# Kernel tuning notes

Measured on AMD Instinct MI355X. Metric: run time of the kernel, lower is better.

The kernel has to match this reference:

```python
import jax, jax.numpy as jnp
import numpy as np

N_ITEM_SRC = 100000
N_ITEM_DST = 50000
N_USER0 = 50000
N_USER1 = 25000
E_II = 800000
E_IU0 = 800000
E_IU1 = 400000
D_IN = 256
D_H = 256
D_OUT = 128


def setup_inputs() -> dict:
    key = jax.random.key(0)
    ks = jax.random.split(key, 16)
    f = jnp.float32
    s = 0.05  # weight init scale
    return {
        "x_item": jax.random.normal(ks[0], (N_ITEM_SRC, D_IN), f),
        "x_user": jax.random.normal(ks[1], (N_USER0, D_H), f),
        "src_ii": jax.random.randint(ks[2], (E_II,), 0, N_ITEM_SRC, jnp.int32),
        "dst_ii": jax.random.randint(ks[3], (E_II,), 0, N_ITEM_DST, jnp.int32),
        "src_iu0": jax.random.randint(ks[4], (E_IU0,), 0, N_ITEM_SRC, jnp.int32),
        "dst_iu0": jax.random.randint(ks[5], (E_IU0,), 0, N_USER0, jnp.int32),
        "src_iu1": jax.random.randint(ks[6], (E_IU1,), 0, N_ITEM_DST, jnp.int32),
        "dst_iu1": jax.random.randint(ks[7], (E_IU1,), 0, N_USER1, jnp.int32),
        "Wn1": jax.random.normal(ks[8], (D_IN, D_H), f) * s,
        "Ws1": jax.random.normal(ks[9], (D_IN, D_H), f) * s,
        "b1": jnp.zeros((D_H,), f),
        "Wn2": jax.random.normal(ks[10], (D_H, D_H), f) * s,
        "Ws2": jax.random.normal(ks[11], (D_H, D_H), f) * s,
        "b2": jnp.zeros((D_H,), f),
        "Wn3": jax.random.normal(ks[12], (D_H, D_H), f) * s,
        "Ws3": jax.random.normal(ks[13], (D_H, D_H), f) * s,
        "b3": jnp.zeros((D_H,), f),
        "Wlin": jax.random.normal(ks[14], (D_H, D_OUT), f) * s,
        "blin": jnp.zeros((D_OUT,), f),
        "n_item_dst": N_ITEM_DST,
        "n_user1": N_USER1,
    }


def _sage_mean(x_src, x_dst, src, dst, n_dst, Wn, Ws, b):
    """DGL SAGEConv('mean'): fc_self(x_dst) + fc_neigh(mean_{in-nbrs} x_src) + bias.
    Isolated dst nodes get zero neighbor contribution (clamp degree to 1)."""
    deg = jax.ops.segment_sum(jnp.ones(dst.shape, x_src.dtype), dst, num_segments=n_dst)
    agg = jax.ops.segment_sum(x_src[src], dst, num_segments=n_dst)  # [n_dst, d]
    agg = agg / jnp.maximum(deg, 1.0)[:, None]
    return x_dst @ Ws + agg @ Wn + b


def reference(x_item, x_user, src_ii, dst_ii, src_iu0, dst_iu0, src_iu1, dst_iu1,
              Wn1, Ws1, b1, Wn2, Ws2, b2, Wn3, Ws3, b3, Wlin, blin,
              n_item_dst, n_user1):
    # conv1: item->item (block: dst item feats are prefix of src item feats)
    item_x = jax.nn.relu(_sage_mean(x_item, x_item[:n_item_dst], src_ii, dst_ii,
                                    n_item_dst, Wn1, Ws1, b1))
    # conv2: item->user at hop 0
    user_x = jax.nn.relu(_sage_mean(x_item, x_user, src_iu0, dst_iu0,
                                    x_user.shape[0], Wn2, Ws2, b2))
    user_x = user_x[:n_user1]
    # conv3: item->user at hop 1
    user_x = jax.nn.relu(_sage_mean(item_x, user_x, src_iu1, dst_iu1,
                                    n_user1, Wn3, Ws3, b3))
    return user_x @ Wlin + blin
```

## Files before the change

kernel.cpp:

```cpp
#include <hip/hip_runtime.h>

#define D 256
#define NI_SRC 100000
#define NI_DST 50000
#define NU1 25000
#define EII 800000
#define EIU0 800000
#define EIU1 400000
#define DOUT 128
#define CAP 60

typedef __bf16 bf16x8 __attribute__((ext_vector_type(8)));
typedef float f32x4 __attribute__((ext_vector_type(4)));

__device__ __forceinline__ unsigned short f2bf(float x) {
    unsigned u = __builtin_bit_cast(unsigned, x);
    u += 0x7FFFu + ((u >> 16) & 1u);
    return (unsigned short)(u >> 16);
}
__device__ __forceinline__ float bflo(unsigned u) { return __builtin_bit_cast(float, u << 16); }
__device__ __forceinline__ float bfhi(unsigned u) { return __builtin_bit_cast(float, u & 0xFFFF0000u); }

__global__ __launch_bounds__(256) void cvt_kernel(const float* __restrict__ in,
                                                  unsigned short* __restrict__ out, long n8) {
    long i = (long)blockIdx.x * blockDim.x + threadIdx.x;
    if (i >= n8) return;
    const float4 f1 = *reinterpret_cast<const float4*>(in + i * 8);
    const float4 f2 = *reinterpret_cast<const float4*>(in + i * 8 + 4);
    uint4 v;
    v.x = f2bf(f1.x) | ((unsigned)f2bf(f1.y) << 16);
    v.y = f2bf(f1.z) | ((unsigned)f2bf(f1.w) << 16);
    v.z = f2bf(f2.x) | ((unsigned)f2bf(f2.y) << 16);
    v.w = f2bf(f2.z) | ((unsigned)f2bf(f2.w) << 16);
    *reinterpret_cast<uint4*>(out + i * 8) = v;
}

__global__ __launch_bounds__(256) void wcvt_all(const float* __restrict__ W0, const float* __restrict__ W1,
                                                const float* __restrict__ W2, const float* __restrict__ W3,
                                                const float* __restrict__ W4, const float* __restrict__ W5,
                                                const float* __restrict__ W6,
                                                unsigned short* __restrict__ out) {
    int t = blockIdx.x * blockDim.x + threadIdx.x;
    const float* W; int NN; int base;
    if (t < 393216) {
        int w = t >> 16; base = w << 16;
        W = (w == 0) ? W0 : (w == 1) ? W1 : (w == 2) ? W2 : (w == 3) ? W3 : (w == 4) ? W4 : W5;
        NN = 256;
    } else if (t < 425984) { base = 393216; W = W6; NN = 128; }
    else return;
    int i = t - base;
    int n = i >> 8, k = i & 255;
    out[t] = f2bf(W[(size_t)k * NN + n]);
}

__global__ void bucket_all(const int* __restrict__ s1, const int* __restrict__ d1,
                           int* __restrict__ u1, int* __restrict__ e1,
                           const int* __restrict__ s2, const int* __restrict__ d2,
                           int* __restrict__ u2, int* __restrict__ e2,
                           const int* __restrict__ s3, const int* __restrict__ d3,
                           int* __restrict__ u3, int* __restrict__ e3) {
    int i0 = blockIdx.x * blockDim.x + threadIdx.x;
    int stride = gridDim.x * blockDim.x;
    for (int i = i0; i < EII; i += stride) {
        int d = d1[i]; int p = atomicAdd(&u1[d], 1);
        if (p < CAP) e1[d * CAP + p] = s1[i];
    }
    for (int i = i0; i < EIU0; i += stride) {
        int d = d2[i];
        if (d < NU1) { int p = atomicAdd(&u2[d], 1); if (p < CAP) e2[d * CAP + p] = s2[i]; }
    }
    for (int i = i0; i < EIU1; i += stride) {
        int d = d3[i]; int p = atomicAdd(&u3[d], 1);
        if (p < CAP) e3[d * CAP + p] = s3[i];
    }
}

__global__ __launch_bounds__(256) void gather_cap(const unsigned short* __restrict__ X,
                                                  const int* __restrict__ csr,
                                                  const int* __restrict__ cnt,
                                                  unsigned short* __restrict__ out, int nrows) {
    int wid = (blockIdx.x * blockDim.x + threadIdx.x) >> 6;
    int lane = threadIdx.x & 63;
    if (wid >= nrows) return;
    int c = min(cnt[wid], CAP);
    const int s = wid * CAP;
    const int half = lane >> 5;
    const int l32 = lane & 31;
    float acc[8] = {};
    for (int j = 0; j < c; j += 64) {
        int myid = (j + lane < c) ? csr[s + j + lane] : 0;
        int rem = min(64, c - j);
        int tmax = min(32, rem);
        for (int t = 0; t < tmax; ++t) {
            int idx = t + half * 32;
            int sid = __shfl(myid, idx, 64);
            if (idx < rem) {
                const uint4 v = *reinterpret_cast<const uint4*>(X + (size_t)sid * D + l32 * 8);
                acc[0] += bflo(v.x); acc[1] += bfhi(v.x);
                acc[2] += bflo(v.y); acc[3] += bfhi(v.y);
                acc[4] += bflo(v.z); acc[5] += bfhi(v.z);
                acc[6] += bflo(v.w); acc[7] += bfhi(v.w);
            }
        }
    }
#pragma unroll
    for (int q = 0; q < 8; ++q) acc[q] += __shfl_xor(acc[q], 32, 64);
    if (half == 0) {
        float r = 1.0f / fmaxf((float)c, 1.0f);
        uint4 o;
        o.x = f2bf(acc[0] * r) | ((unsigned)f2bf(acc[1] * r) << 16);
        o.y = f2bf(acc[2] * r) | ((unsigned)f2bf(acc[3] * r) << 16);
        o.z = f2bf(acc[4] * r) | ((unsigned)f2bf(acc[5] * r) << 16);
        o.w = f2bf(acc[6] * r) | ((unsigned)f2bf(acc[7] * r) << 16);
        *reinterpret_cast<uint4*>(out + (size_t)wid * D + l32 * 8) = o;
    }
}

template<bool A1F32, bool HAS_AGG, bool RELU, bool OUTF32>
__global__ __launch_bounds__(256) void sage_gemm(
    const unsigned short* __restrict__ A1b, const float* __restrict__ A1f,
    const unsigned short* __restrict__ A2,
    const unsigned short* __restrict__ W1t, const unsigned short* __restrict__ W2t,
    const float* __restrict__ bias,
    unsigned short* __restrict__ Cb, float* __restrict__ Cf,
    int M, int N)
{
    __shared__ unsigned short sA[128 * 40];
    __shared__ unsigned short sB[128 * 40];
    const int tid = threadIdx.x;
    const int lane = tid & 63;
    const int wid = tid >> 6;
    const int wrow = (wid >> 1) * 64;
    const int wcol = (wid & 1) * 64;
    const int brow = blockIdx.x * 128;
    const int bcol = blockIdx.y * 128;

    f32x4 acc[4][4] = {};

    const int r0 = tid >> 2;
    const int k0 = (tid & 3) * 8;

    const int nPass = HAS_AGG ? 2 : 1;
    for (int pass = 0; pass < nPass; ++pass) {
        const unsigned short* __restrict__ Wt = pass ? W2t : W1t;
        for (int kt = 0; kt < 256; kt += 32) {
#pragma unroll
            for (int c = 0; c < 2; ++c) {
                int row = r0 + c * 64;
                int grow = brow + row;
                uint4 val = {0u, 0u, 0u, 0u};
                if (pass == 0) {
                    if (A1F32) {
                        if (grow < M) {
                            const float4 f1 = *reinterpret_cast<const float4*>(A1f + (size_t)grow * 256 + kt + k0);
                            const float4 f2 = *reinterpret_cast<const float4*>(A1f + (size_t)grow * 256 + kt + k0 + 4);
                            val.x = f2bf(f1.x) | ((unsigned)f2bf(f1.y) << 16);
                            val.y = f2bf(f1.z) | ((unsigned)f2bf(f1.w) << 16);
                            val.z = f2bf(f2.x) | ((unsigned)f2bf(f2.y) << 16);
                            val.w = f2bf(f2.z) | ((unsigned)f2bf(f2.w) << 16);
                        }
                    } else {
                        if (grow < M) val = *reinterpret_cast<const uint4*>(A1b + (size_t)grow * 256 + kt + k0);
                    }
                } else {
                    if (grow < M) val = *reinterpret_cast<const uint4*>(A2 + (size_t)grow * 256 + kt + k0);
                }
                *reinterpret_cast<uint4*>(sA + row * 40 + k0) = val;
                *reinterpret_cast<uint4*>(sB + row * 40 + k0) =
                    *reinterpret_cast<const uint4*>(Wt + (size_t)(bcol + row) * 256 + kt + k0);
            }
            __syncthreads();
            const int fr = lane & 15;
            const int fk = (lane >> 4) * 8;
            bf16x8 af[4], bfr[4];
#pragma unroll
            for (int f = 0; f < 4; ++f) {
                af[f]  = __builtin_bit_cast(bf16x8, *reinterpret_cast<const uint4*>(sA + (wrow + f * 16 + fr) * 40 + fk));
                bfr[f] = __builtin_bit_cast(bf16x8, *reinterpret_cast<const uint4*>(sB + (wcol + f * 16 + fr) * 40 + fk));
            }
#pragma unroll
            for (int mi = 0; mi < 4; ++mi)
#pragma unroll
                for (int ni = 0; ni < 4; ++ni)
                    acc[mi][ni] = __builtin_amdgcn_mfma_f32_16x16x32_bf16(af[mi], bfr[ni], acc[mi][ni], 0, 0, 0);
            __syncthreads();
        }
    }

    const int cr = (lane >> 4) * 4;
    const int cc = lane & 15;
#pragma unroll
    for (int mi = 0; mi < 4; ++mi) {
#pragma unroll
        for (int j = 0; j < 4; ++j) {
            int grow = brow + wrow + mi * 16 + cr + j;
            if (grow >= M) continue;
#pragma unroll
            for (int ni = 0; ni < 4; ++ni) {
                int gcol = bcol + wcol + ni * 16 + cc;
                float v = acc[mi][ni][j] + bias[gcol];
                if (RELU) v = fmaxf(v, 0.f);
                if (OUTF32) Cf[(size_t)grow * N + gcol] = v;
                else Cb[(size_t)grow * N + gcol] = f2bf(v);
            }
        }
    }
}

extern "C" void kernel_launch(void* const* d_in, const int* in_sizes, int n_in,
                              void* d_out, int out_size, void* d_ws, size_t ws_size,
                              hipStream_t stream) {
    const float* x_item = (const float*)d_in[0];
    const float* x_user = (const float*)d_in[1];
    const int* src_ii  = (const int*)d_in[2];
    const int* dst_ii  = (const int*)d_in[3];
    const int* src_iu0 = (const int*)d_in[4];
    const int* dst_iu0 = (const int*)d_in[5];
    const int* src_iu1 = (const int*)d_in[6];
    const int* dst_iu1 = (const int*)d_in[7];
    const float* Wn1 = (const float*)d_in[8];
    const float* Ws1 = (const float*)d_in[9];
    const float* b1  = (const float*)d_in[10];
    const float* Wn2 = (const float*)d_in[11];
    const float* Ws2 = (const float*)d_in[12];
    const float* b2  = (const float*)d_in[13];
    const float* Wn3 = (const float*)d_in[14];
    const float* Ws3 = (const float*)d_in[15];
    const float* b3  = (const float*)d_in[16];
    const float* Wlin = (const float*)d_in[17];
    const float* blin = (const float*)d_in[18];
    float* out = (float*)d_out;

    unsigned short* xb_item = (unsigned short*)d_ws;
    unsigned short* aggbuf  = xb_item + (size_t)NI_SRC * D;
    unsigned short* item_x  = aggbuf + (size_t)NI_DST * D;
    unsigned short* wts     = item_x + (size_t)NI_DST * D;
    unsigned short* overlay = wts + 425984;

    unsigned short* user_x2 = overlay;
    int* cur1 = (int*)overlay;
    int* cur2 = cur1 + 50000;
    int* cur3 = cur2 + 25000;
    int* csr1 = cur3 + 25000;
    int* csr2 = csr1 + 50000 * CAP;
    int* csr3 = csr2 + 25000 * CAP;

    unsigned short* Wt_s1 = wts;
    unsigned short* Wt_n1 = wts + 65536;
    unsigned short* Wt_s2 = wts + 2 * 65536;
    unsigned short* Wt_n2 = wts + 3 * 65536;
    unsigned short* Wt_s3 = wts + 4 * 65536;
    unsigned short* Wt_n3 = wts + 5 * 65536;
    unsigned short* Wt_li = wts + 6 * 65536;

    unsigned short* agg2 = aggbuf;
    unsigned short* agg3 = aggbuf + (size_t)NU1 * D;
    unsigned short* user_x3 = aggbuf;

    long n8 = (long)NI_SRC * D / 8;
    cvt_kernel<<<(int)((n8 + 255) / 256), 256, 0, stream>>>(x_item, xb_item, n8);
    wcvt_all<<<1664, 256, 0, stream>>>(Ws1, Wn1, Ws2, Wn2, Ws3, Wn3, Wlin, wts);

    hipMemsetAsync(cur1, 0, sizeof(int) * 100000, stream);
    bucket_all<<<512, 256, 0, stream>>>(src_ii, dst_ii, cur1, csr1,
                                        src_iu0, dst_iu0, cur2, csr2,
                                        src_iu1, dst_iu1, cur3, csr3);

    dim3 g1((NI_DST + 127) / 128, 2);
    dim3 g2((NU1 + 127) / 128, 2);
    dim3 g4((NU1 + 127) / 128, 1);

    gather_cap<<<(NI_DST * 64 + 255) / 256, 256, 0, stream>>>(xb_item, csr1, cur1, aggbuf, NI_DST);
    sage_gemm<false, true, true, false><<<g1, 256, 0, stream>>>(
        xb_item, nullptr, aggbuf, Wt_s1, Wt_n1, b1, item_x, nullptr, NI_DST, D);

    gather_cap<<<(NU1 * 64 + 255) / 256, 256, 0, stream>>>(xb_item, csr2, cur2, agg2, NU1);
    gather_cap<<<(NU1 * 64 + 255) / 256, 256, 0, stream>>>(item_x, csr3, cur3, agg3, NU1);

    sage_gemm<true, true, true, false><<<g2, 256, 0, stream>>>(
        nullptr, x_user, agg2, Wt_s2, Wt_n2, b2, user_x2, nullptr, NU1, D);

    sage_gemm<false, true, true, false><<<g2, 256, 0, stream>>>(
        user_x2, nullptr, agg3, Wt_s3, Wt_n3, b3, user_x3, nullptr, NU1, D);

    sage_gemm<false, false, false, true><<<g4, 256, 0, stream>>>(
        user_x3, nullptr, nullptr, Wt_li, nullptr, blin, nullptr, out, NU1, DOUT);
}
```

Measured before the change: 389.6 us.

## Merge independent prep, gather and GEMM stages into combined launches

Three preprocessing kernels (edge bucketing, weight transpose-convert and feature bf16 conversion) become one block-partitioned prep kernel, and the bucketing now loads edges eight at a time with int4 loads. The conv1 and conv2 neighbour gathers are merged into one launch, and so are their two GEMMs. Conv1's self term now reads the fp32 features directly. Workspace buffers are re-overlaid so the merged stages can share memory. The aim is fewer launches and less tail idle time between small dependent kernels, at the cost of uneven work mixes inside a single grid.

```diff
diff --git a/kernel.cpp b/kernel.cpp
--- a/kernel.cpp
+++ b/kernel.cpp
@@ -10,6 +10,14 @@
 #define DOUT 128
 #define CAP 60
 
+#define NB_BUCKET 512
+#define NB_WCVT 1664
+#define NB_CVT 12500
+#define NGRP1 100000
+#define NGRP2 100000
+#define NGRP3 50000
+#define NGRP 250000
+
 typedef __bf16 bf16x8 __attribute__((ext_vector_type(8)));
 typedef float f32x4 __attribute__((ext_vector_type(4)));
 
@@ -21,66 +29,67 @@
 __device__ __forceinline__ float bflo(unsigned u) { return __builtin_bit_cast(float, u << 16); }
 __device__ __forceinline__ float bfhi(unsigned u) { return __builtin_bit_cast(float, u & 0xFFFF0000u); }
 
-__global__ __launch_bounds__(256) void cvt_kernel(const float* __restrict__ in,
-                                                  unsigned short* __restrict__ out, long n8) {
-    long i = (long)blockIdx.x * blockDim.x + threadIdx.x;
-    if (i >= n8) return;
-    const float4 f1 = *reinterpret_cast<const float4*>(in + i * 8);
-    const float4 f2 = *reinterpret_cast<const float4*>(in + i * 8 + 4);
-    uint4 v;
-    v.x = f2bf(f1.x) | ((unsigned)f2bf(f1.y) << 16);
-    v.y = f2bf(f1.z) | ((unsigned)f2bf(f1.w) << 16);
-    v.z = f2bf(f2.x) | ((unsigned)f2bf(f2.y) << 16);
-    v.w = f2bf(f2.z) | ((unsigned)f2bf(f2.w) << 16);
-    *reinterpret_cast<uint4*>(out + i * 8) = v;
-}
-
-__global__ __launch_bounds__(256) void wcvt_all(const float* __restrict__ W0, const float* __restrict__ W1,
-                                                const float* __restrict__ W2, const float* __restrict__ W3,
-                                                const float* __restrict__ W4, const float* __restrict__ W5,
-                                                const float* __restrict__ W6,
-                                                unsigned short* __restrict__ out) {
-    int t = blockIdx.x * blockDim.x + threadIdx.x;
-    const float* W; int NN; int base;
-    if (t < 393216) {
-        int w = t >> 16; base = w << 16;
-        W = (w == 0) ? W0 : (w == 1) ? W1 : (w == 2) ? W2 : (w == 3) ? W3 : (w == 4) ? W4 : W5;
-        NN = 256;
-    } else if (t < 425984) { base = 393216; W = W6; NN = 128; }
-    else return;
-    int i = t - base;
-    int n = i >> 8, k = i & 255;
-    out[t] = f2bf(W[(size_t)k * NN + n]);
-}
-
-__global__ void bucket_all(const int* __restrict__ s1, const int* __restrict__ d1,
-                           int* __restrict__ u1, int* __restrict__ e1,
-                           const int* __restrict__ s2, const int* __restrict__ d2,
-                           int* __restrict__ u2, int* __restrict__ e2,
-                           const int* __restrict__ s3, const int* __restrict__ d3,
-                           int* __restrict__ u3, int* __restrict__ e3) {
-    int i0 = blockIdx.x * blockDim.x + threadIdx.x;
-    int stride = gridDim.x * blockDim.x;
-    for (int i = i0; i < EII; i += stride) {
-        int d = d1[i]; int p = atomicAdd(&u1[d], 1);
-        if (p < CAP) e1[d * CAP + p] = s1[i];
-    }
-    for (int i = i0; i < EIU0; i += stride) {
-        int d = d2[i];
-        if (d < NU1) { int p = atomicAdd(&u2[d], 1); if (p < CAP) e2[d * CAP + p] = s2[i]; }
-    }
-    for (int i = i0; i < EIU1; i += stride) {
-        int d = d3[i]; int p = atomicAdd(&u3[d], 1);
-        if (p < CAP) e3[d * CAP + p] = s3[i];
-    }
-}
-
-__global__ __launch_bounds__(256) void gather_cap(const unsigned short* __restrict__ X,
-                                                  const int* __restrict__ csr,
-                                                  const int* __restrict__ cnt,
-                                                  unsigned short* __restrict__ out, int nrows) {
-    int wid = (blockIdx.x * blockDim.x + threadIdx.x) >> 6;
-    int lane = threadIdx.x & 63;
+__device__ __forceinline__ void bucket8(const int* __restrict__ src, const int* __restrict__ dst,
+                                        int* __restrict__ cur, int* __restrict__ csr, int g, int dmax) {
+    const int4 da = reinterpret_cast<const int4*>(dst)[g * 2];
+    const int4 db = reinterpret_cast<const int4*>(dst)[g * 2 + 1];
+    const int4 sa = reinterpret_cast<const int4*>(src)[g * 2];
+    const int4 sb = reinterpret_cast<const int4*>(src)[g * 2 + 1];
+    int d[8] = {da.x, da.y, da.z, da.w, db.x, db.y, db.z, db.w};
+    int s[8] = {sa.x, sa.y, sa.z, sa.w, sb.x, sb.y, sb.z, sb.w};
+    int p[8];
+#pragma unroll
+    for (int q = 0; q < 8; ++q) p[q] = (d[q] < dmax) ? atomicAdd(&cur[d[q]], 1) : CAP;
+#pragma unroll
+    for (int q = 0; q < 8; ++q) if (p[q] < CAP) csr[d[q] * CAP + p[q]] = s[q];
+}
+
+__global__ __launch_bounds__(256) void prep_kernel(
+    const int* __restrict__ s1, const int* __restrict__ d1, int* __restrict__ u1, int* __restrict__ e1,
+    const int* __restrict__ s2, const int* __restrict__ d2, int* __restrict__ u2, int* __restrict__ e2,
+    const int* __restrict__ s3, const int* __restrict__ d3, int* __restrict__ u3, int* __restrict__ e3,
+    const float* __restrict__ W0, const float* __restrict__ W1, const float* __restrict__ W2,
+    const float* __restrict__ W3, const float* __restrict__ W4, const float* __restrict__ W5,
+    const float* __restrict__ W6, unsigned short* __restrict__ wout,
+    const float* __restrict__ xin, unsigned short* __restrict__ xout)
+{
+    int b = blockIdx.x;
+    if (b < NB_BUCKET) {
+        int t0 = b * 256 + threadIdx.x;
+        for (int g = t0; g < NGRP; g += NB_BUCKET * 256) {
+            if (g < NGRP1) bucket8(s1, d1, u1, e1, g, NI_DST);
+            else if (g < NGRP1 + NGRP2) bucket8(s2, d2, u2, e2, g - NGRP1, NU1);
+            else bucket8(s3, d3, u3, e3, g - NGRP1 - NGRP2, NU1);
+        }
+    } else if (b < NB_BUCKET + NB_WCVT) {
+        int t = (b - NB_BUCKET) * 256 + threadIdx.x;
+        const float* W; int NN; int base;
+        if (t < 393216) {
+            int w = t >> 16; base = w << 16;
+            W = (w == 0) ? W0 : (w == 1) ? W1 : (w == 2) ? W2 : (w == 3) ? W3 : (w == 4) ? W4 : W5;
+            NN = 256;
+        } else { base = 393216; W = W6; NN = 128; }
+        int i = t - base;
+        int n = i >> 8, k = i & 255;
+        wout[t] = f2bf(W[(size_t)k * NN + n]);
+    } else {
+        long i = (long)(b - NB_BUCKET - NB_WCVT) * 256 + threadIdx.x;
+        const float4 f1 = *reinterpret_cast<const float4*>(xin + i * 8);
+        const float4 f2 = *reinterpret_cast<const float4*>(xin + i * 8 + 4);
+        uint4 v;
+        v.x = f2bf(f1.x) | ((unsigned)f2bf(f1.y) << 16);
+        v.y = f2bf(f1.z) | ((unsigned)f2bf(f1.w) << 16);
+        v.z = f2bf(f2.x) | ((unsigned)f2bf(f2.y) << 16);
+        v.w = f2bf(f2.z) | ((unsigned)f2bf(f2.w) << 16);
+        *reinterpret_cast<uint4*>(xout + i * 8) = v;
+    }
+}
+
+__device__ __forceinline__ void gather_body(const unsigned short* __restrict__ X,
+                                            const int* __restrict__ csr,
+                                            const int* __restrict__ cnt,
+                                            unsigned short* __restrict__ out,
+                                            int nrows, int wid, int lane) {
     if (wid >= nrows) return;
     int c = min(cnt[wid], CAP);
     const int s = wid * CAP;
@@ -116,8 +125,29 @@
     }
 }
 
+__global__ __launch_bounds__(256) void gather_cap(const unsigned short* __restrict__ X,
+                                                  const int* __restrict__ csr,
+                                                  const int* __restrict__ cnt,
+                                                  unsigned short* __restrict__ out, int nrows) {
+    int wid = (blockIdx.x * blockDim.x + threadIdx.x) >> 6;
+    gather_body(X, csr, cnt, out, nrows, wid, threadIdx.x & 63);
+}
+
+__global__ __launch_bounds__(256) void gather12(const unsigned short* __restrict__ X,
+                                                const int* __restrict__ csr1, const int* __restrict__ cnt1,
+                                                unsigned short* __restrict__ out1,
+                                                const int* __restrict__ csr2, const int* __restrict__ cnt2,
+                                                unsigned short* __restrict__ out2)
+{
+    int wid = (blockIdx.x * blockDim.x + threadIdx.x) >> 6;
+    int lane = threadIdx.x & 63;
+    if (wid < NI_DST) gather_body(X, csr1, cnt1, out1, NI_DST, wid, lane);
+    else gather_body(X, csr2, cnt2, out2, NU1, wid - NI_DST, lane);
+}
+
 template<bool A1F32, bool HAS_AGG, bool RELU, bool OUTF32>
-__global__ __launch_bounds__(256) void sage_gemm(
+__device__ __forceinline__ void gemm_body(
+    int bx, int by, unsigned short* sA, unsigned short* sB,
     const unsigned short* __restrict__ A1b, const float* __restrict__ A1f,
     const unsigned short* __restrict__ A2,
     const unsigned short* __restrict__ W1t, const unsigned short* __restrict__ W2t,
@@ -125,15 +155,13 @@
     unsigned short* __restrict__ Cb, float* __restrict__ Cf,
     int M, int N)
 {
-    __shared__ unsigned short sA[128 * 40];
-    __shared__ unsigned short sB[128 * 40];
     const int tid = threadIdx.x;
     const int lane = tid & 63;
     const int wid = tid >> 6;
     const int wrow = (wid >> 1) * 64;
     const int wcol = (wid & 1) * 64;
-    const int brow = blockIdx.x * 128;
-    const int bcol = blockIdx.y * 128;
+    const int brow = bx * 128;
+    const int bcol = by * 128;
 
     f32x4 acc[4][4] = {};
 
@@ -207,6 +235,42 @@
     }
 }
 
+template<bool A1F32, bool HAS_AGG, bool RELU, bool OUTF32>
+__global__ __launch_bounds__(256) void sage_gemm(
+    const unsigned short* __restrict__ A1b, const float* __restrict__ A1f,
+    const unsigned short* __restrict__ A2,
+    const unsigned short* __restrict__ W1t, const unsigned short* __restrict__ W2t,
+    const float* __restrict__ bias,
+    unsigned short* __restrict__ Cb, float* __restrict__ Cf,
+    int M, int N)
+{
+    __shared__ unsigned short sA[128 * 40];
+    __shared__ unsigned short sB[128 * 40];
+    gemm_body<A1F32, HAS_AGG, RELU, OUTF32>(blockIdx.x, blockIdx.y, sA, sB,
+        A1b, A1f, A2, W1t, W2t, bias, Cb, Cf, M, N);
+}
+
+__global__ __launch_bounds__(256) void gemm12(
+    const float* __restrict__ x_item, const unsigned short* __restrict__ agg1,
+    const unsigned short* __restrict__ Wt_s1, const unsigned short* __restrict__ Wt_n1,
+    const float* __restrict__ b1, unsigned short* __restrict__ item_x, int ng1,
+    const float* __restrict__ x_user, const unsigned short* __restrict__ agg2,
+    const unsigned short* __restrict__ Wt_s2, const unsigned short* __restrict__ Wt_n2,
+    const float* __restrict__ b2, unsigned short* __restrict__ user_x2)
+{
+    __shared__ unsigned short sA[128 * 40];
+    __shared__ unsigned short sB[128 * 40];
+    int b = blockIdx.x;
+    if (b < ng1) {
+        gemm_body<true, true, true, false>(b >> 1, b & 1, sA, sB,
+            nullptr, x_item, agg1, Wt_s1, Wt_n1, b1, item_x, nullptr, NI_DST, 256);
+    } else {
+        int b2i = b - ng1;
+        gemm_body<true, true, true, false>(b2i >> 1, b2i & 1, sA, sB,
+            nullptr, x_user, agg2, Wt_s2, Wt_n2, b2, user_x2, nullptr, NU1, 256);
+    }
+}
+
 extern "C" void kernel_launch(void* const* d_in, const int* in_sizes, int n_in,
                               void* d_out, int out_size, void* d_ws, size_t ws_size,
                               hipStream_t stream) {
@@ -232,18 +296,20 @@
     float* out = (float*)d_out;
 
     unsigned short* xb_item = (unsigned short*)d_ws;
-    unsigned short* aggbuf  = xb_item + (size_t)NI_SRC * D;
-    unsigned short* item_x  = aggbuf + (size_t)NI_DST * D;
-    unsigned short* wts     = item_x + (size_t)NI_DST * D;
-    unsigned short* overlay = wts + 425984;
-
-    unsigned short* user_x2 = overlay;
-    int* cur1 = (int*)overlay;
+    unsigned short* wts     = xb_item + 25600000;
+    unsigned short* agg1    = wts + 425984;
+    unsigned short* agg2    = agg1 + 12800000;
+    int* cur1 = (int*)(agg2 + 6400000);
     int* cur2 = cur1 + 50000;
     int* cur3 = cur2 + 25000;
-    int* csr1 = cur3 + 25000;
-    int* csr2 = csr1 + 50000 * CAP;
-    int* csr3 = csr2 + 25000 * CAP;
+    int* csr3 = cur3 + 25000;
+    unsigned short* item_x = (unsigned short*)(csr3 + 1500000);
+    int* csr2 = (int*)item_x;
+    int* csr1 = csr2 + 1500000;
+
+    unsigned short* user_x2 = xb_item;
+    unsigned short* agg3    = xb_item + 6400000;
+    unsigned short* user_x3 = xb_item + 12800000;
 
     unsigned short* Wt_s1 = wts;
     unsigned short* Wt_n1 = wts + 65536;
@@ -253,36 +319,31 @@
     unsigned short* Wt_n3 = wts + 5 * 65536;
     unsigned short* Wt_li = wts + 6 * 65536;
 
-    unsigned short* agg2 = aggbuf;
-    unsigned short* agg3 = aggbuf + (size_t)NU1 * D;
-    unsigned short* user_x3 = aggbuf;
-
-    long n8 = (long)NI_SRC * D / 8;
-    cvt_kernel<<<(int)((n8 + 255) / 256), 256, 0, stream>>>(x_item, xb_item, n8);
-    wcvt_all<<<1664, 256, 0, stream>>>(Ws1, Wn1, Ws2, Wn2, Ws3, Wn3, Wlin, wts);
-
     hipMemsetAsync(cur1, 0, sizeof(int) * 100000, stream);
-    bucket_all<<<512, 256, 0, stream>>>(src_ii, dst_ii, cur1, csr1,
-                                        src_iu0, dst_iu0, cur2, csr2,
-                                        src_iu1, dst_iu1, cur3, csr3);
-
-    dim3 g1((NI_DST + 127) / 128, 2);
+
+    prep_kernel<<<NB_BUCKET + NB_WCVT + NB_CVT, 256, 0, stream>>>(
+        src_ii, dst_ii, cur1, csr1,
+        src_iu0, dst_iu0, cur2, csr2,
+        src_iu1, dst_iu1, cur3, csr3,
+        Ws1, Wn1, Ws2, Wn2, Ws3, Wn3, Wlin, wts,
+        x_item, xb_item);
+
+    gather12<<<(NI_DST + NU1) * 64 / 256, 256, 0, stream>>>(
+        xb_item, csr1, cur1, agg1, csr2, cur2, agg2);
+
+    const int ng1 = ((NI_DST + 127) / 128) * 2;
+    const int ng2 = ((NU1 + 127) / 128) * 2;
+    gemm12<<<ng1 + ng2, 256, 0, stream>>>(
+        x_item, agg1, Wt_s1, Wt_n1, b1, item_x, ng1,
+        x_user, agg2, Wt_s2, Wt_n2, b2, user_x2);
+
+    gather_cap<<<(NU1 * 64) / 256, 256, 0, stream>>>(item_x, csr3, cur3, agg3, NU1);
+
     dim3 g2((NU1 + 127) / 128, 2);
-    dim3 g4((NU1 + 127) / 128, 1);
-
-    gather_cap<<<(NI_DST * 64 + 255) / 256, 256, 0, stream>>>(xb_item, csr1, cur1, aggbuf, NI_DST);
-    sage_gemm<false, true, true, false><<<g1, 256, 0, stream>>>(
-        xb_item, nullptr, aggbuf, Wt_s1, Wt_n1, b1, item_x, nullptr, NI_DST, D);
-
-    gather_cap<<<(NU1 * 64 + 255) / 256, 256, 0, stream>>>(xb_item, csr2, cur2, agg2, NU1);
-    gather_cap<<<(NU1 * 64 + 255) / 256, 256, 0, stream>>>(item_x, csr3, cur3, agg3, NU1);
-
-    sage_gemm<true, true, true, false><<<g2, 256, 0, stream>>>(
-        nullptr, x_user, agg2, Wt_s2, Wt_n2, b2, user_x2, nullptr, NU1, D);
-
     sage_gemm<false, true, true, false><<<g2, 256, 0, stream>>>(
         user_x2, nullptr, agg3, Wt_s3, Wt_n3, b3, user_x3, nullptr, NU1, D);
 
+    dim3 g4((NU1 + 127) / 128, 1);
     sage_gemm<false, false, false, true><<<g4, 256, 0, stream>>>(
         user_x3, nullptr, nullptr, Wt_li, nullptr, blin, nullptr, out, NU1, DOUT);
 }
```

Result: faster. 378.1 us (-2.9%).
